# Optimization experiments

Hardware: AMD Instinct MI355X
Metric: run time of the kernel (lower is better)

## Reference

```python
import jax, jax.numpy as jnp
import numpy as np

B, T, C, H, W = 2, 8, 512, 32, 32
HEADS, HD = 8, 64          # head_dim = C // num_heads
GROUPS = 32                # GroupNorm_0 num_groups
EPS = 1e-6


def setup_inputs() -> dict:
    key = jax.random.key(0)
    k = jax.random.split(key, 5)
    return {
        "x": jax.random.normal(k[0], (B, T, C, H, W), jnp.float32),
        "gn_scale": jnp.ones((C,), jnp.float32),
        "gn_bias": jnp.zeros((C,), jnp.float32),
        "w_qkv": jax.random.normal(k[1], (C, 3 * C), jnp.float32) / float(np.sqrt(C)),
        "b_qkv": jnp.zeros((3 * C,), jnp.float32),
        "w_out": jax.random.normal(k[2], (C, C), jnp.float32) / float(np.sqrt(C)),
        "b_out": jnp.zeros((C,), jnp.float32),
    }


def reference(x, gn_scale, gn_bias, w_qkv, b_qkv, w_out, b_out):
    Bv, Tv, Cv, Hv, Wv = x.shape
    N = Bv * Tv
    xv = x.reshape(N, Cv, Hv, Wv)

    # GroupNorm(32 groups, eps=1e-6) with affine
    g = xv.reshape(N, GROUPS, Cv // GROUPS, Hv, Wv)
    mu = g.mean(axis=(2, 3, 4), keepdims=True)
    var = g.var(axis=(2, 3, 4), keepdims=True)
    hn = ((g - mu) * jax.lax.rsqrt(var + EPS)).reshape(N, Cv, Hv, Wv)
    hn = hn * gn_scale[None, :, None, None] + gn_bias[None, :, None, None]

    # NIN qkv projection (per-pixel 1x1): (N,C,H,W) x (C,3C) -> (N,3C,H,W)
    h = jnp.einsum('nchw,cd->ndhw', hn, w_qkv) + b_qkv[None, :, None, None]
    h = h.reshape(N, HEADS, 3 * HD, Hv * Wv).transpose(0, 1, 3, 2)  # (N,h,S,3d)
    q, k, v = jnp.split(h, 3, axis=-1)

    # naive scaled dot-product attention over S = H*W tokens
    logits = jnp.einsum('nhsd,nhtd->nhst', q, k) / float(np.sqrt(HD))
    attn = jax.nn.softmax(logits, axis=-1)
    vals = jnp.einsum('nhst,nhtd->nhsd', attn, v)

    h = vals.transpose(0, 1, 3, 2).reshape(N, Cv, Hv, Wv)
    # output NIN (init_scale=0 in torch; random params here) + residual
    h = jnp.einsum('nchw,cd->ndhw', h, w_out) + b_out[None, :, None, None]
    return x + h.reshape(Bv, Tv, Cv, Hv, Wv)
```

## Files before the change

kernel.cpp:

```cpp
#include <hip/hip_runtime.h>
#include <stdint.h>

typedef __bf16 bf16x8 __attribute__((ext_vector_type(8)));
typedef float f32x4v __attribute__((ext_vector_type(4)));
typedef float f32x16v __attribute__((ext_vector_type(16)));
typedef unsigned u32x2 __attribute__((ext_vector_type(2)));

__device__ __forceinline__ unsigned f2bf_rn(float f) {
    return (__float_as_uint(f) + 0x8000u) >> 16;
}
__device__ __forceinline__ unsigned pk2bf(float a, float b) {
    return __builtin_amdgcn_perm(__float_as_uint(b) + 0x8000u,
                                 __float_as_uint(a) + 0x8000u, 0x07060302u);
}

__device__ __forceinline__ void swap32(unsigned &a, unsigned &b) {
#if __has_builtin(__builtin_amdgcn_permlane32_swap)
    u32x2 r = __builtin_amdgcn_permlane32_swap(a, b, false, false);
    a = r[0]; b = r[1];
#else
    unsigned pa = (unsigned)__shfl_xor((int)a, 32);
    unsigned pb = (unsigned)__shfl_xor((int)b, 32);
    bool hi = (threadIdx.x & 32) != 0;
    unsigned na = hi ? pb : a;
    unsigned nb = hi ? b : pa;
    a = na; b = nb;
#endif
}

__device__ __forceinline__ bf16x8 mk8(unsigned a, unsigned b, unsigned c, unsigned e) {
    union { int4 i; bf16x8 v; } u;
    u.i = make_int4((int)a, (int)b, (int)c, (int)e);
    return u.v;
}

#define GLD_LDS16(gp, lp) __builtin_amdgcn_global_load_lds( \
    (const __attribute__((address_space(1))) unsigned int*)(gp), \
    (__attribute__((address_space(3))) unsigned int*)(lp), 16, 0, 0)

__global__ __launch_bounds__(256) void wt_kernel(const float* __restrict__ wqkv,
        const float* __restrict__ wout, unsigned short* __restrict__ WqT,
        unsigned short* __restrict__ WoT) {
    __shared__ float tile[32][33];
    int bx = blockIdx.x;
    const float* in; unsigned short* out; int Cc, c0;
    if (bx < 48) { in = wqkv; out = WqT; Cc = 1536; c0 = bx * 32; }
    else         { in = wout; out = WoT; Cc = 512;  c0 = (bx - 48) * 32; }
    int r0 = blockIdx.y * 32;
    int tx = threadIdx.x & 31, ty = threadIdx.x >> 5;
    #pragma unroll
    for (int i = 0; i < 4; i++) {
        int r = ty + i * 8;
        tile[r][tx] = in[(size_t)(r0 + r) * Cc + c0 + tx];
    }
    __syncthreads();
    #pragma unroll
    for (int i = 0; i < 4; i++) {
        int cr = ty + i * 8;
        out[(size_t)(c0 + cr) * 512 + r0 + tx] = (unsigned short)f2bf_rn(tile[tx][cr]);
    }
}

__global__ __launch_bounds__(256) void gn_kernel(const float* __restrict__ x,
        const float* __restrict__ scale, const float* __restrict__ bias,
        unsigned short* __restrict__ hnT) {
    int blk = blockIdx.x;
    int tid = threadIdx.x;
    int g = blk & 31, n = blk >> 5;
    const float4* src4 = (const float4*)(x + (size_t)blk * 16384);

    float s = 0.f, s2 = 0.f;
    for (int i = tid; i < 4096; i += 256) {
        float4 v = src4[i];
        s  += v.x + v.y + v.z + v.w;
        s2 += v.x*v.x + v.y*v.y + v.z*v.z + v.w*v.w;
    }
    __shared__ float red[256], red2[256];
    red[tid] = s; red2[tid] = s2;
    __syncthreads();
    for (int off = 128; off > 0; off >>= 1) {
        if (tid < off) { red[tid] += red[tid+off]; red2[tid] += red2[tid+off]; }
        __syncthreads();
    }
    __shared__ float sc_s[16], bi_s[16];
    if (tid < 16) {
        float mean = red[0] * (1.f/16384.f);
        float var  = red2[0] * (1.f/16384.f) - mean*mean;
        float rstd = rsqrtf(var + 1e-6f);
        int c = g*16 + tid;
        float sc = scale[c] * rstd;
        sc_s[tid] = sc;
        bi_s[tid] = bias[c] - mean * sc;
    }
    __shared__ float tile[16][260];
    for (int ch = 0; ch < 4; ch++) {
        __syncthreads();
        #pragma unroll
        for (int kk = 0; kk < 4; kk++) {
            int fi = tid + kk*256;
            int row = fi >> 6, col4 = fi & 63;
            float4 v = src4[row*256 + ch*64 + col4];
            *(float4*)&tile[row][col4*4] = v;
        }
        __syncthreads();
        int sQ = ch*256 + tid;
        unsigned int pk[8];
        #pragma unroll
        for (int c2 = 0; c2 < 8; c2++) {
            float a = tile[c2*2][tid]   * sc_s[c2*2]   + bi_s[c2*2];
            float b = tile[c2*2+1][tid] * sc_s[c2*2+1] + bi_s[c2*2+1];
            pk[c2] = pk2bf(a, b);
        }
        unsigned short* op = hnT + ((size_t)(n*1024 + sQ))*512 + g*16;
        *(uint4*)op       = make_uint4(pk[0], pk[1], pk[2], pk[3]);
        *((uint4*)op + 1) = make_uint4(pk[4], pk[5], pk[6], pk[7]);
    }
}

__global__ __launch_bounds__(256) void qkv_kernel(
        const unsigned short* __restrict__ WqT, const unsigned short* __restrict__ hnT,
        const float* __restrict__ bqkv,
        unsigned short* __restrict__ qb, unsigned short* __restrict__ kbuf,
        unsigned short* __restrict__ vb) {
    int s0 = blockIdx.x * 128, m0 = blockIdx.y * 128, n = blockIdx.z;
    __shared__ unsigned short At[4096];
    __shared__ unsigned short Bt[4096];
    int tid = threadIdx.x;
    int lane = tid & 63, w = tid >> 6;
    int quad = lane >> 4, tx = lane & 15;
    int moff = (w & 1) * 64, soff = (w >> 1) * 64;

    const unsigned short* Arow = WqT + (size_t)m0 * 512;
    const unsigned short* Brow = hnT + ((size_t)n * 1024 + s0) * 512;

    f32x4v acc[4][4];
    #pragma unroll
    for (int i = 0; i < 4; i++)
        #pragma unroll
        for (int j = 0; j < 4; j++)
            #pragma unroll
            for (int e = 0; e < 4; e++) acc[i][j][e] = 0.f;

    int f1 = tid, f2 = tid + 256;
    int m1 = f1 >> 2, kb1 = ((f1 & 3) - (f1 >> 3)) & 3;
    int m2 = f2 >> 2, kb2 = ((f2 & 3) - (f2 >> 3)) & 3;

    for (int k0 = 0; k0 < 512; k0 += 32) {
        __syncthreads();
        GLD_LDS16(Arow + (size_t)m1*512 + k0 + kb1*8, At + f1*8);
        GLD_LDS16(Arow + (size_t)m2*512 + k0 + kb2*8, At + f2*8);
        GLD_LDS16(Brow + (size_t)m1*512 + k0 + kb1*8, Bt + f1*8);
        GLD_LDS16(Brow + (size_t)m2*512 + k0 + kb2*8, Bt + f2*8);
        __syncthreads();
        bf16x8 af[4], bfr[4];
        #pragma unroll
        for (int mt = 0; mt < 4; mt++) {
            int m = moff + mt*16 + tx;
            int ch = m*4 + ((quad + (m >> 1)) & 3);
            af[mt] = *(const bf16x8*)(At + ch*8);
        }
        #pragma unroll
        for (int nt = 0; nt < 4; nt++) {
            int m = soff + nt*16 + tx;
            int ch = m*4 + ((quad + (m >> 1)) & 3);
            bfr[nt] = *(const bf16x8*)(Bt + ch*8);
        }
        #pragma unroll
        for (int mt = 0; mt < 4; mt++)
            #pragma unroll
            for (int nt = 0; nt < 4; nt++)
                acc[mt][nt] = __builtin_amdgcn_mfma_f32_16x16x32_bf16(
                    af[mt], bfr[nt], acc[mt][nt], 0, 0, 0);
    }

    const float QSCL = 0.18033688011112042f;
    #pragma unroll
    for (int mt = 0; mt < 4; mt++) {
        int m = m0 + moff + mt*16 + quad*4;
        int head = m / 192;
        int r = m - head*192;
        int which = r >> 6;
        int d0 = r & 63;
        float4 bia = *(const float4*)(bqkv + m);
        float scl = (which == 0) ? QSCL : 1.0f;
        #pragma unroll
        for (int nt = 0; nt < 4; nt++) {
            int sQ = s0 + soff + nt*16 + tx;
            f32x4v a = acc[mt][nt];
            float v0 = (a[0]+bia.x)*scl, v1 = (a[1]+bia.y)*scl;
            float v2 = (a[2]+bia.z)*scl, v3 = (a[3]+bia.w)*scl;
            if (which < 2) {
                unsigned short* base = (which == 0) ? qb : kbuf;
                unsigned lo = pk2bf(v0, v1), hi2 = pk2bf(v2, v3);
                *(uint2*)(base + (((size_t)(n*8 + head)*1024 + sQ) << 6) + d0) =
                    make_uint2(lo, hi2);
            } else {
                size_t vbase = ((size_t)(n*8 + head)*64 + d0)*1024 + sQ;
                vb[vbase]        = (unsigned short)f2bf_rn(v0);
                vb[vbase + 1024] = (unsigned short)f2bf_rn(v1);
                vb[vbase + 2048] = (unsigned short)f2bf_rn(v2);
                vb[vbase + 3072] = (unsigned short)f2bf_rn(v3);
            }
        }
    }
}

__global__ __launch_bounds__(256) void attn_kernel(
        const unsigned short* __restrict__ qg, const unsigned short* __restrict__ kg,
        const unsigned short* __restrict__ vg, unsigned short* __restrict__ ao) {
    int bid = blockIdx.x;
    int nh = bid & 127, qbk = bid >> 7;
    int tid = threadIdx.x, w = tid >> 6, lane = tid & 63;
    int lq = lane & 31, hi = lane >> 5;
    const unsigned short* Q = qg + (size_t)nh * 65536;
    const unsigned short* K = kg + (size_t)nh * 65536;
    const unsigned short* V = vg + (size_t)nh * 65536;

    __shared__ unsigned short Klds[2][64*72];
    __shared__ unsigned short Vlds[2][64*72];
    __shared__ float lsum_s[4][32];

    int q0 = qbk*128 + w*32;
    bf16x8 qf[4];
    #pragma unroll
    for (int ks = 0; ks < 4; ks++)
        qf[ks] = *(const bf16x8*)(Q + ((size_t)(q0 + lq))*64 + ks*16 + hi*8);

    int r = tid >> 2, part = (tid & 3) * 16;
    uint4 ka, kb2, va, vb2;
    ka  = *(const uint4*)(K + (size_t)r*64 + part);
    kb2 = *(const uint4*)(K + (size_t)r*64 + part + 8);
    va  = *(const uint4*)(V + (size_t)r*1024 + part);
    vb2 = *(const uint4*)(V + (size_t)r*1024 + part + 8);

    f32x16v O0, O1;
    #pragma unroll
    for (int i = 0; i < 16; i++) { O0[i] = 0.f; O1[i] = 0.f; }
    float lsum = 0.f;

    for (int it = 0; it < 16; it++) {
        int buf = it & 1;
        {
            unsigned short* kd = Klds[buf] + r*72 + part;
            *(uint4*)kd = ka; *(uint4*)(kd+8) = kb2;
            unsigned short* vd = Vlds[buf] + r*72 + part;
            *(uint4*)vd = va; *(uint4*)(vd+8) = vb2;
        }
        __syncthreads();
        if (it < 15) {
            int t0 = (it + 1) * 64;
            ka  = *(const uint4*)(K + (size_t)(t0 + r)*64 + part);
            kb2 = *(const uint4*)(K + (size_t)(t0 + r)*64 + part + 8);
            va  = *(const uint4*)(V + (size_t)r*1024 + t0 + part);
            vb2 = *(const uint4*)(V + (size_t)r*1024 + t0 + part + 8);
        }
        const unsigned short* Kb = Klds[buf];
        const unsigned short* Vb = Vlds[buf];

        f32x16v S0, S1;
        #pragma unroll
        for (int i = 0; i < 16; i++) { S0[i] = 0.f; S1[i] = 0.f; }
        #pragma unroll
        for (int ks = 0; ks < 4; ks++) {
            bf16x8 a0 = *(const bf16x8*)(Kb + lq*72 + ks*16 + hi*8);
            bf16x8 a1 = *(const bf16x8*)(Kb + (32+lq)*72 + ks*16 + hi*8);
            S0 = __builtin_amdgcn_mfma_f32_32x32x16_bf16(a0, qf[ks], S0, 0, 0, 0);
            S1 = __builtin_amdgcn_mfma_f32_32x32x16_bf16(a1, qf[ks], S1, 0, 0, 0);
        }

        #pragma unroll
        for (int i = 0; i < 16; i++) {
            S0[i] = exp2f(S0[i]);
            S1[i] = exp2f(S1[i]);
            lsum += S0[i] + S1[i];
        }
        unsigned d[16];
        #pragma unroll
        for (int p2 = 0; p2 < 8; p2++) {
            d[p2]     = pk2bf(S0[p2*2], S0[p2*2+1]);
            d[8 + p2] = pk2bf(S1[p2*2], S1[p2*2+1]);
        }
        swap32(d[0],  d[2]);  swap32(d[1],  d[3]);
        swap32(d[4],  d[6]);  swap32(d[5],  d[7]);
        swap32(d[8],  d[10]); swap32(d[9],  d[11]);
        swap32(d[12], d[14]); swap32(d[13], d[15]);

        #pragma unroll
        for (int kc = 0; kc < 4; kc++) {
            bf16x8 pa = mk8(d[kc*4+0], d[kc*4+1], d[kc*4+2], d[kc*4+3]);
            bf16x8 v0 = *(const bf16x8*)(Vb + lq*72 + kc*16 + hi*8);
            bf16x8 v1 = *(const bf16x8*)(Vb + (32+lq)*72 + kc*16 + hi*8);
            O0 = __builtin_amdgcn_mfma_f32_32x32x16_bf16(pa, v0, O0, 0, 0, 0);
            O1 = __builtin_amdgcn_mfma_f32_32x32x16_bf16(pa, v1, O1, 0, 0, 0);
        }
    }

    lsum += __shfl_xor(lsum, 32);
    lsum_s[w][lq] = lsum;
    int n = nh >> 3, h = nh & 7;
    #pragma unroll
    for (int rq = 0; rq < 4; rq++) {
        float4 lv = *(const float4*)&lsum_s[w][rq*8 + hi*4];
        float invs[4] = {1.f/lv.x, 1.f/lv.y, 1.f/lv.z, 1.f/lv.w};
        #pragma unroll
        for (int i = 0; i < 4; i++) {
            int sQ = q0 + rq*8 + hi*4 + i;
            size_t rowb = ((size_t)(n*1024 + sQ))*512 + h*64;
            ao[rowb + lq]      = (unsigned short)f2bf_rn(O0[rq*4+i] * invs[i]);
            ao[rowb + 32 + lq] = (unsigned short)f2bf_rn(O1[rq*4+i] * invs[i]);
        }
    }
}

__global__ __launch_bounds__(256) void out_kernel(
        const unsigned short* __restrict__ aoT, const unsigned short* __restrict__ WoT,
        const float* __restrict__ bout, const float* __restrict__ x,
        float* __restrict__ out) {
    int s0 = blockIdx.x * 128, d0b = blockIdx.y * 128, n = blockIdx.z;
    __shared__ unsigned short At[4096];
    __shared__ unsigned short Bt[4096];
    int tid = threadIdx.x;
    int lane = tid & 63, w = tid >> 6;
    int quad = lane >> 4, tx = lane & 15;
    int moff = (w & 1) * 64, noff = (w >> 1) * 64;

    const unsigned short* Arow = aoT + ((size_t)n * 1024 + s0) * 512;
    const unsigned short* Brow = WoT + (size_t)d0b * 512;

    f32x4v acc[4][4];
    #pragma unroll
    for (int i = 0; i < 4; i++)
        #pragma unroll
        for (int j = 0; j < 4; j++)
            #pragma unroll
            for (int e = 0; e < 4; e++) acc[i][j][e] = 0.f;

    int f1 = tid, f2 = tid + 256;
    int m1 = f1 >> 2, kb1 = ((f1 & 3) - (f1 >> 3)) & 3;
    int m2 = f2 >> 2, kb2 = ((f2 & 3) - (f2 >> 3)) & 3;

    for (int k0 = 0; k0 < 512; k0 += 32) {
        __syncthreads();
        GLD_LDS16(Arow + (size_t)m1*512 + k0 + kb1*8, At + f1*8);
        GLD_LDS16(Arow + (size_t)m2*512 + k0 + kb2*8, At + f2*8);
        GLD_LDS16(Brow + (size_t)m1*512 + k0 + kb1*8, Bt + f1*8);
        GLD_LDS16(Brow + (size_t)m2*512 + k0 + kb2*8, Bt + f2*8);
        __syncthreads();
        bf16x8 af[4], bfr[4];
        #pragma unroll
        for (int mt = 0; mt < 4; mt++) {
            int m = moff + mt*16 + tx;
            int ch = m*4 + ((quad + (m >> 1)) & 3);
            af[mt] = *(const bf16x8*)(At + ch*8);
        }
        #pragma unroll
        for (int nt = 0; nt < 4; nt++) {
            int m = noff + nt*16 + tx;
            int ch = m*4 + ((quad + (m >> 1)) & 3);
            bfr[nt] = *(const bf16x8*)(Bt + ch*8);
        }
        #pragma unroll
        for (int mt = 0; mt < 4; mt++)
            #pragma unroll
            for (int nt = 0; nt < 4; nt++)
                acc[mt][nt] = __builtin_amdgcn_mfma_f32_16x16x32_bf16(
                    af[mt], bfr[nt], acc[mt][nt], 0, 0, 0);
    }

    #pragma unroll
    for (int mt = 0; mt < 4; mt++) {
        int sQ = s0 + moff + mt*16 + quad*4;
        #pragma unroll
        for (int nt = 0; nt < 4; nt++) {
            int d = d0b + noff + nt*16 + tx;
            float bo = bout[d];
            size_t base = ((size_t)n*512 + d)*1024 + sQ;
            float4 xv = *(const float4*)(x + base);
            f32x4v a = acc[mt][nt];
            float4 o = make_float4(a[0]+bo+xv.x, a[1]+bo+xv.y, a[2]+bo+xv.z, a[3]+bo+xv.w);
            *(float4*)(out + base) = o;
        }
    }
}

extern "C" void kernel_launch(void* const* d_in, const int* in_sizes, int n_in,
                              void* d_out, int out_size, void* d_ws, size_t ws_size,
                              hipStream_t stream) {
    const float* x    = (const float*)d_in[0];
    const float* gns  = (const float*)d_in[1];
    const float* gnb  = (const float*)d_in[2];
    const float* wqkv = (const float*)d_in[3];
    const float* bqkv = (const float*)d_in[4];
    const float* wout = (const float*)d_in[5];
    const float* bout = (const float*)d_in[6];
    float* out = (float*)d_out;

    char* p = (char*)d_ws;
    size_t off = 0;
    auto carve = [&](size_t bytes) {
        char* r = p + off;
        off = (off + bytes + 255) & ~(size_t)255;
        return r;
    };
    unsigned short* hnT = (unsigned short*)carve((size_t)16*1024*512*2);
    unsigned short* qb2 = (unsigned short*)carve((size_t)128*1024*64*2);
    unsigned short* kb2 = (unsigned short*)carve((size_t)128*1024*64*2);
    unsigned short* vb2 = (unsigned short*)carve((size_t)128*64*1024*2);
    unsigned short* aoT = (unsigned short*)carve((size_t)16*1024*512*2);
    unsigned short* WqT = (unsigned short*)carve((size_t)1536*512*2);
    unsigned short* WoT = (unsigned short*)carve((size_t)512*512*2);

    wt_kernel<<<dim3(64, 16), 256, 0, stream>>>(wqkv, wout, WqT, WoT);
    gn_kernel<<<dim3(512), 256, 0, stream>>>(x, gns, gnb, hnT);
    qkv_kernel<<<dim3(8, 12, 16), 256, 0, stream>>>(WqT, hnT, bqkv, qb2, kb2, vb2);
    attn_kernel<<<dim3(1024), 256, 0, stream>>>(qb2, kb2, vb2, aoT);
    out_kernel<<<dim3(8, 4, 16), 256, 0, stream>>>(aoT, WoT, bout, x, out);
}
```

Before: 238.8 us.

## Double query rows per attention wave and merge weight-transpose into GroupNorm launch

```diff
diff --git a/kernel.cpp b/kernel.cpp
--- a/kernel.cpp
+++ b/kernel.cpp
@@ -38,34 +38,39 @@
     (const __attribute__((address_space(1))) unsigned int*)(gp), \
     (__attribute__((address_space(3))) unsigned int*)(lp), 16, 0, 0)
 
-__global__ __launch_bounds__(256) void wt_kernel(const float* __restrict__ wqkv,
-        const float* __restrict__ wout, unsigned short* __restrict__ WqT,
-        unsigned short* __restrict__ WoT) {
-    __shared__ float tile[32][33];
-    int bx = blockIdx.x;
-    const float* in; unsigned short* out; int Cc, c0;
-    if (bx < 48) { in = wqkv; out = WqT; Cc = 1536; c0 = bx * 32; }
-    else         { in = wout; out = WoT; Cc = 512;  c0 = (bx - 48) * 32; }
-    int r0 = blockIdx.y * 32;
-    int tx = threadIdx.x & 31, ty = threadIdx.x >> 5;
-    #pragma unroll
-    for (int i = 0; i < 4; i++) {
-        int r = ty + i * 8;
-        tile[r][tx] = in[(size_t)(r0 + r) * Cc + c0 + tx];
-    }
-    __syncthreads();
-    #pragma unroll
-    for (int i = 0; i < 4; i++) {
-        int cr = ty + i * 8;
-        out[(size_t)(c0 + cr) * 512 + r0 + tx] = (unsigned short)f2bf_rn(tile[tx][cr]);
-    }
-}
-
-__global__ __launch_bounds__(256) void gn_kernel(const float* __restrict__ x,
+__global__ __launch_bounds__(256) void prep_kernel(const float* __restrict__ x,
         const float* __restrict__ scale, const float* __restrict__ bias,
-        unsigned short* __restrict__ hnT) {
-    int blk = blockIdx.x;
+        unsigned short* __restrict__ hnT,
+        const float* __restrict__ wqkv, const float* __restrict__ wout,
+        unsigned short* __restrict__ WqT, unsigned short* __restrict__ WoT) {
+    __shared__ float red[256], red2[256];
+    __shared__ float sc_s[16], bi_s[16];
+    __shared__ float tile[16][260];
+    __shared__ float wtile[32][33];
+    int bid = blockIdx.x;
     int tid = threadIdx.x;
+    if (bid >= 512) {
+        int b2 = bid - 512;
+        int bx = b2 & 63, by = b2 >> 6;
+        const float* in; unsigned short* out; int Cc, c0;
+        if (bx < 48) { in = wqkv; out = WqT; Cc = 1536; c0 = bx * 32; }
+        else         { in = wout; out = WoT; Cc = 512;  c0 = (bx - 48) * 32; }
+        int r0 = by * 32;
+        int tx = tid & 31, ty = tid >> 5;
+        #pragma unroll
+        for (int i = 0; i < 4; i++) {
+            int r = ty + i * 8;
+            wtile[r][tx] = in[(size_t)(r0 + r) * Cc + c0 + tx];
+        }
+        __syncthreads();
+        #pragma unroll
+        for (int i = 0; i < 4; i++) {
+            int cr = ty + i * 8;
+            out[(size_t)(c0 + cr) * 512 + r0 + tx] = (unsigned short)f2bf_rn(wtile[tx][cr]);
+        }
+        return;
+    }
+    int blk = bid;
     int g = blk & 31, n = blk >> 5;
     const float4* src4 = (const float4*)(x + (size_t)blk * 16384);
 
@@ -75,14 +80,12 @@
         s  += v.x + v.y + v.z + v.w;
         s2 += v.x*v.x + v.y*v.y + v.z*v.z + v.w*v.w;
     }
-    __shared__ float red[256], red2[256];
     red[tid] = s; red2[tid] = s2;
     __syncthreads();
     for (int off = 128; off > 0; off >>= 1) {
         if (tid < off) { red[tid] += red[tid+off]; red2[tid] += red2[tid+off]; }
         __syncthreads();
     }
-    __shared__ float sc_s[16], bi_s[16];
     if (tid < 16) {
         float mean = red[0] * (1.f/16384.f);
         float var  = red2[0] * (1.f/16384.f) - mean*mean;
@@ -92,7 +95,6 @@
         sc_s[tid] = sc;
         bi_s[tid] = bias[c] - mean * sc;
     }
-    __shared__ float tile[16][260];
     for (int ch = 0; ch < 4; ch++) {
         __syncthreads();
         #pragma unroll
@@ -218,13 +220,15 @@
 
     __shared__ unsigned short Klds[2][64*72];
     __shared__ unsigned short Vlds[2][64*72];
-    __shared__ float lsum_s[4][32];
-
-    int q0 = qbk*128 + w*32;
-    bf16x8 qf[4];
-    #pragma unroll
-    for (int ks = 0; ks < 4; ks++)
-        qf[ks] = *(const bf16x8*)(Q + ((size_t)(q0 + lq))*64 + ks*16 + hi*8);
+    __shared__ float lsum_s[4][64];
+
+    int q0 = qbk*256 + w*64;
+    bf16x8 qfA[4], qfB[4];
+    #pragma unroll
+    for (int ks = 0; ks < 4; ks++) {
+        qfA[ks] = *(const bf16x8*)(Q + ((size_t)(q0 + lq))*64      + ks*16 + hi*8);
+        qfB[ks] = *(const bf16x8*)(Q + ((size_t)(q0 + 32 + lq))*64 + ks*16 + hi*8);
+    }
 
     int r = tid >> 2, part = (tid & 3) * 16;
     uint4 ka, kb2, va, vb2;
@@ -233,10 +237,10 @@
     va  = *(const uint4*)(V + (size_t)r*1024 + part);
     vb2 = *(const uint4*)(V + (size_t)r*1024 + part + 8);
 
-    f32x16v O0, O1;
-    #pragma unroll
-    for (int i = 0; i < 16; i++) { O0[i] = 0.f; O1[i] = 0.f; }
-    float lsum = 0.f;
+    f32x16v OA0, OA1, OB0, OB1;
+    #pragma unroll
+    for (int i = 0; i < 16; i++) { OA0[i]=0.f; OA1[i]=0.f; OB0[i]=0.f; OB1[i]=0.f; }
+    float lsumA = 0.f, lsumB = 0.f;
 
     for (int it = 0; it < 16; it++) {
         int buf = it & 1;
@@ -257,57 +261,101 @@
         const unsigned short* Kb = Klds[buf];
         const unsigned short* Vb = Vlds[buf];
 
-        f32x16v S0, S1;
-        #pragma unroll
-        for (int i = 0; i < 16; i++) { S0[i] = 0.f; S1[i] = 0.f; }
-        #pragma unroll
-        for (int ks = 0; ks < 4; ks++) {
-            bf16x8 a0 = *(const bf16x8*)(Kb + lq*72 + ks*16 + hi*8);
-            bf16x8 a1 = *(const bf16x8*)(Kb + (32+lq)*72 + ks*16 + hi*8);
-            S0 = __builtin_amdgcn_mfma_f32_32x32x16_bf16(a0, qf[ks], S0, 0, 0, 0);
-            S1 = __builtin_amdgcn_mfma_f32_32x32x16_bf16(a1, qf[ks], S1, 0, 0, 0);
-        }
-
-        #pragma unroll
-        for (int i = 0; i < 16; i++) {
-            S0[i] = exp2f(S0[i]);
-            S1[i] = exp2f(S1[i]);
-            lsum += S0[i] + S1[i];
-        }
-        unsigned d[16];
-        #pragma unroll
-        for (int p2 = 0; p2 < 8; p2++) {
-            d[p2]     = pk2bf(S0[p2*2], S0[p2*2+1]);
-            d[8 + p2] = pk2bf(S1[p2*2], S1[p2*2+1]);
-        }
-        swap32(d[0],  d[2]);  swap32(d[1],  d[3]);
-        swap32(d[4],  d[6]);  swap32(d[5],  d[7]);
-        swap32(d[8],  d[10]); swap32(d[9],  d[11]);
-        swap32(d[12], d[14]); swap32(d[13], d[15]);
-
-        #pragma unroll
-        for (int kc = 0; kc < 4; kc++) {
-            bf16x8 pa = mk8(d[kc*4+0], d[kc*4+1], d[kc*4+2], d[kc*4+3]);
-            bf16x8 v0 = *(const bf16x8*)(Vb + lq*72 + kc*16 + hi*8);
-            bf16x8 v1 = *(const bf16x8*)(Vb + (32+lq)*72 + kc*16 + hi*8);
-            O0 = __builtin_amdgcn_mfma_f32_32x32x16_bf16(pa, v0, O0, 0, 0, 0);
-            O1 = __builtin_amdgcn_mfma_f32_32x32x16_bf16(pa, v1, O1, 0, 0, 0);
-        }
-    }
-
-    lsum += __shfl_xor(lsum, 32);
-    lsum_s[w][lq] = lsum;
+        {
+            f32x16v S0, S1;
+            #pragma unroll
+            for (int i = 0; i < 16; i++) { S0[i] = 0.f; S1[i] = 0.f; }
+            #pragma unroll
+            for (int ks = 0; ks < 4; ks++) {
+                bf16x8 a0 = *(const bf16x8*)(Kb + lq*72 + ks*16 + hi*8);
+                bf16x8 a1 = *(const bf16x8*)(Kb + (32+lq)*72 + ks*16 + hi*8);
+                S0 = __builtin_amdgcn_mfma_f32_32x32x16_bf16(a0, qfA[ks], S0, 0, 0, 0);
+                S1 = __builtin_amdgcn_mfma_f32_32x32x16_bf16(a1, qfA[ks], S1, 0, 0, 0);
+            }
+            #pragma unroll
+            for (int i = 0; i < 16; i++) {
+                S0[i] = exp2f(S0[i]);
+                S1[i] = exp2f(S1[i]);
+                lsumA += S0[i] + S1[i];
+            }
+            unsigned d[16];
+            #pragma unroll
+            for (int p2 = 0; p2 < 8; p2++) {
+                d[p2]     = pk2bf(S0[p2*2], S0[p2*2+1]);
+                d[8 + p2] = pk2bf(S1[p2*2], S1[p2*2+1]);
+            }
+            swap32(d[0],  d[2]);  swap32(d[1],  d[3]);
+            swap32(d[4],  d[6]);  swap32(d[5],  d[7]);
+            swap32(d[8],  d[10]); swap32(d[9],  d[11]);
+            swap32(d[12], d[14]); swap32(d[13], d[15]);
+            #pragma unroll
+            for (int kc = 0; kc < 4; kc++) {
+                bf16x8 pa = mk8(d[kc*4+0], d[kc*4+1], d[kc*4+2], d[kc*4+3]);
+                bf16x8 v0 = *(const bf16x8*)(Vb + lq*72 + kc*16 + hi*8);
+                bf16x8 v1 = *(const bf16x8*)(Vb + (32+lq)*72 + kc*16 + hi*8);
+                OA0 = __builtin_amdgcn_mfma_f32_32x32x16_bf16(pa, v0, OA0, 0, 0, 0);
+                OA1 = __builtin_amdgcn_mfma_f32_32x32x16_bf16(pa, v1, OA1, 0, 0, 0);
+            }
+        }
+        {
+            f32x16v S0, S1;
+            #pragma unroll
+            for (int i = 0; i < 16; i++) { S0[i] = 0.f; S1[i] = 0.f; }
+            #pragma unroll
+            for (int ks = 0; ks < 4; ks++) {
+                bf16x8 a0 = *(const bf16x8*)(Kb + lq*72 + ks*16 + hi*8);
+                bf16x8 a1 = *(const bf16x8*)(Kb + (32+lq)*72 + ks*16 + hi*8);
+                S0 = __builtin_amdgcn_mfma_f32_32x32x16_bf16(a0, qfB[ks], S0, 0, 0, 0);
+                S1 = __builtin_amdgcn_mfma_f32_32x32x16_bf16(a1, qfB[ks], S1, 0, 0, 0);
+            }
+            #pragma unroll
+            for (int i = 0; i < 16; i++) {
+                S0[i] = exp2f(S0[i]);
+                S1[i] = exp2f(S1[i]);
+                lsumB += S0[i] + S1[i];
+            }
+            unsigned d[16];
+            #pragma unroll
+            for (int p2 = 0; p2 < 8; p2++) {
+                d[p2]     = pk2bf(S0[p2*2], S0[p2*2+1]);
+                d[8 + p2] = pk2bf(S1[p2*2], S1[p2*2+1]);
+            }
+            swap32(d[0],  d[2]);  swap32(d[1],  d[3]);
+            swap32(d[4],  d[6]);  swap32(d[5],  d[7]);
+            swap32(d[8],  d[10]); swap32(d[9],  d[11]);
+            swap32(d[12], d[14]); swap32(d[13], d[15]);
+            #pragma unroll
+            for (int kc = 0; kc < 4; kc++) {
+                bf16x8 pa = mk8(d[kc*4+0], d[kc*4+1], d[kc*4+2], d[kc*4+3]);
+                bf16x8 v0 = *(const bf16x8*)(Vb + lq*72 + kc*16 + hi*8);
+                bf16x8 v1 = *(const bf16x8*)(Vb + (32+lq)*72 + kc*16 + hi*8);
+                OB0 = __builtin_amdgcn_mfma_f32_32x32x16_bf16(pa, v0, OB0, 0, 0, 0);
+                OB1 = __builtin_amdgcn_mfma_f32_32x32x16_bf16(pa, v1, OB1, 0, 0, 0);
+            }
+        }
+    }
+
+    lsumA += __shfl_xor(lsumA, 32);
+    lsumB += __shfl_xor(lsumB, 32);
+    lsum_s[w][lq] = lsumA;
+    lsum_s[w][32 + lq] = lsumB;
     int n = nh >> 3, h = nh & 7;
     #pragma unroll
     for (int rq = 0; rq < 4; rq++) {
-        float4 lv = *(const float4*)&lsum_s[w][rq*8 + hi*4];
-        float invs[4] = {1.f/lv.x, 1.f/lv.y, 1.f/lv.z, 1.f/lv.w};
+        float4 lvA = *(const float4*)&lsum_s[w][rq*8 + hi*4];
+        float4 lvB = *(const float4*)&lsum_s[w][32 + rq*8 + hi*4];
+        float invA[4] = {1.f/lvA.x, 1.f/lvA.y, 1.f/lvA.z, 1.f/lvA.w};
+        float invB[4] = {1.f/lvB.x, 1.f/lvB.y, 1.f/lvB.z, 1.f/lvB.w};
         #pragma unroll
         for (int i = 0; i < 4; i++) {
-            int sQ = q0 + rq*8 + hi*4 + i;
-            size_t rowb = ((size_t)(n*1024 + sQ))*512 + h*64;
-            ao[rowb + lq]      = (unsigned short)f2bf_rn(O0[rq*4+i] * invs[i]);
-            ao[rowb + 32 + lq] = (unsigned short)f2bf_rn(O1[rq*4+i] * invs[i]);
+            int sA = q0 + rq*8 + hi*4 + i;
+            size_t rowA = ((size_t)(n*1024 + sA))*512 + h*64;
+            ao[rowA + lq]      = (unsigned short)f2bf_rn(OA0[rq*4+i] * invA[i]);
+            ao[rowA + 32 + lq] = (unsigned short)f2bf_rn(OA1[rq*4+i] * invA[i]);
+            int sB = sA + 32;
+            size_t rowB = ((size_t)(n*1024 + sB))*512 + h*64;
+            ao[rowB + lq]      = (unsigned short)f2bf_rn(OB0[rq*4+i] * invB[i]);
+            ao[rowB + 32 + lq] = (unsigned short)f2bf_rn(OB1[rq*4+i] * invB[i]);
         }
     }
 }
@@ -410,9 +458,8 @@
     unsigned short* WqT = (unsigned short*)carve((size_t)1536*512*2);
     unsigned short* WoT = (unsigned short*)carve((size_t)512*512*2);
 
-    wt_kernel<<<dim3(64, 16), 256, 0, stream>>>(wqkv, wout, WqT, WoT);
-    gn_kernel<<<dim3(512), 256, 0, stream>>>(x, gns, gnb, hnT);
+    prep_kernel<<<dim3(1536), 256, 0, stream>>>(x, gns, gnb, hnT, wqkv, wout, WqT, WoT);
     qkv_kernel<<<dim3(8, 12, 16), 256, 0, stream>>>(WqT, hnT, bqkv, qb2, kb2, vb2);
-    attn_kernel<<<dim3(1024), 256, 0, stream>>>(qb2, kb2, vb2, aoT);
+    attn_kernel<<<dim3(512), 256, 0, stream>>>(qb2, kb2, vb2, aoT);
     out_kernel<<<dim3(8, 4, 16), 256, 0, stream>>>(aoT, WoT, bout, x, out);
 }
```

New measurement: 248.1 us. +3.9%, slower.
